# Optimization experiments

Measured on AMD Instinct MI355X. Metric: run time of the kernel, lower is better.

The kernel has to match this reference:

```python
import jax, jax.numpy as jnp
import numpy as np

B, C, H, W_SP = 32, 128, 56, 56
OC, K, STRIDE, PAD = 256, 3, 1, 1


def setup_inputs() -> dict:
    key = jax.random.key(0)
    k1, k2, k3 = jax.random.split(key, 3)
    x = jax.random.normal(k1, (B, C, H, W_SP), dtype=jnp.float32)
    # nn.Linear weight: [out_features, in_features] = [OC, C*K*K]
    W = jax.random.normal(k2, (OC, C * K * K), dtype=jnp.float32) * 0.02
    b = jax.random.normal(k3, (OC,), dtype=jnp.float32) * 0.02
    return {"x": x, "W": W, "b": b}


def reference(x, W, b):
    # The torch module does im2col (unfold+permute+reshape) then Linear.
    # Patch layout after view/permute is (C, kh, kw) flattened, so the
    # Linear weight reshaped to [OC, C, K, K] is exactly an OIHW conv
    # kernel; direct convolution computes identical math without
    # materializing the im2col tensor.
    kernel = W.reshape(OC, C, K, K)
    out = jax.lax.conv_general_dilated(
        x, kernel,
        window_strides=(STRIDE, STRIDE),
        padding=[(PAD, PAD), (PAD, PAD)],
        dimension_numbers=("NCHW", "OIHW", "NCHW"),
    )
    return out + b[None, :, None, None]
```

## Files before the change

kernel.cpp:

```cpp
#include <hip/hip_runtime.h>
#include <hip/hip_bf16.h>
#include <stdint.h>

typedef unsigned short u16;
typedef unsigned int   u32;
typedef __bf16 bf16x8 __attribute__((ext_vector_type(8)));
typedef float  f32x4  __attribute__((ext_vector_type(4)));

#define BATCH 32
#define CIN   128
#define HH    56
#define WW    56
#define OC    256
#define HP    58
#define WP    58
#define PLANE  (HH*WW)
#define KDIM   1152
#define NKT    36

#define XPAD_ELEMS (BATCH*HP*WP*CIN)
#define W3_ELEMS   (OC*KDIM)

#define GLDS16(g, l) __builtin_amdgcn_global_load_lds( \
    (const __attribute__((address_space(1))) void*)(g), \
    (__attribute__((address_space(3))) void*)(l), 16, 0, 0)

__global__ void zero_ws(uint4* __restrict__ p, int n4) {
    int i = blockIdx.x * blockDim.x + threadIdx.x;
    if (i < n4) p[i] = (uint4){0, 0, 0, 0};
}

__global__ __launch_bounds__(256) void pad_tr(const float* __restrict__ x,
                                              u16* __restrict__ xpad) {
    __shared__ u16 T16[56 * 130];
    const int h = blockIdx.x;
    const int b = blockIdx.y;
    const int tid = threadIdx.x;

    const float* src = x + (size_t)b * CIN * PLANE + h * WW;
#pragma unroll
    for (int j = 0; j < 28; ++j) {
        int flat = j * 256 + tid;
        int c = flat / 56;
        int w = flat - c * 56;
        float v = src[(size_t)c * PLANE + w];
        __hip_bfloat16 bv = __float2bfloat16(v);
        T16[w * 130 + c] = *(u16*)&bv;
    }
    __syncthreads();

    const u32* T32 = (const u32*)T16;
    uint4* dst = (uint4*)(xpad + ((size_t)(b * HP + h + 1) * WP + 1) * CIN);
#pragma unroll
    for (int j = 0; j < 4; ++j) {
        int g = j * 256 + tid;
        if (g < 896) {
            int wp = g >> 4, cq = g & 15;
            uint4 v;
            v.x = T32[wp * 65 + cq * 4 + 0];
            v.y = T32[wp * 65 + cq * 4 + 1];
            v.z = T32[wp * 65 + cq * 4 + 2];
            v.w = T32[wp * 65 + cq * 4 + 3];
            dst[g] = v;
        }
    }
}

__global__ void pack_w(const float* __restrict__ W, u16* __restrict__ w3) {
    int o = blockIdx.x * blockDim.x + threadIdx.x;
    if (o >= W3_ELEMS) return;
    int nt   = o / (NKT * 4096);
    int rem  = o - nt * (NKT * 4096);
    int kt   = rem / 4096;
    int rem2 = rem - kt * 4096;
    int ni   = rem2 >> 5;
    int ci   = rem2 & 31;
    int n = nt * 128 + ni;
    int r = kt >> 2;
    int c = ((kt & 3) << 5) + ci;
    float val = W[n * KDIM + c * 9 + r];
    __hip_bfloat16 bv = __float2bfloat16(val);
    w3[o] = *(u16*)&bv;
}

__global__ __launch_bounds__(256) void conv_main(
    const u16* __restrict__ xpad,
    const u16* __restrict__ w3,
    const float* __restrict__ bias,
    float* __restrict__ out)
{
    __shared__ __align__(16) u16 As[128 * 32];
    __shared__ __align__(16) u16 Bs[128 * 32];

    const int tid  = threadIdx.x;
    const int lane = tid & 63;
    const int wv   = tid >> 6;
    const int m0   = blockIdx.x * 128;
    const int nt   = blockIdx.y;

    const int mi0 = wv * 32 + (lane >> 2);
    size_t bbase[2];
#pragma unroll
    for (int i = 0; i < 2; ++i) {
        int mi = mi0 + i * 16;
        int m  = m0 + mi;
        int bb = m / PLANE;
        int s  = m - bb * PLANE;
        int hh = s / WW;
        int ww = s - hh * WW;
        bbase[i] = ((size_t)((bb * HP + hh) * WP + ww) * CIN + (lane & 3) * 8) * 2;
    }
    const char* w3t  = (const char*)(w3 + (size_t)nt * (NKT * 4096));
    const size_t abase = (size_t)(wv * 128 + lane) * 16;

    char* AsW = (char*)As + wv * 2048;
    char* BsW = (char*)Bs + wv * 2048;

    const int wn = wv >> 1, wm = wv & 1;
    const int l16 = lane & 15, quad = lane >> 4;

    f32x4 acc[4][4];
#pragma unroll
    for (int f = 0; f < 4; ++f) {
        f32x4 bv = *(const f32x4*)&bias[nt * 128 + wn * 64 + f * 16 + quad * 4];
#pragma unroll
        for (int g = 0; g < 4; ++g) acc[f][g] = bv;
    }

    for (int r = 0; r < 9; ++r) {
        const int kh = (r * 11) >> 5;
        const int kw = r - kh * 3;
        const size_t xoff = (size_t)(kh * WP + kw) * CIN * 2;
#pragma unroll
        for (int cc = 0; cc < 4; ++cc) {
            const int kt = r * 4 + cc;
#pragma unroll
            for (int i = 0; i < 2; ++i) {
                GLDS16(w3t + (size_t)kt * 8192 + abase + i * 1024,
                       AsW + i * 1024);
                GLDS16((const char*)xpad + bbase[i] + xoff + cc * 64,
                       BsW + i * 1024);
            }
            __syncthreads();

            bf16x8 af[4], bfr[4];
#pragma unroll
            for (int f = 0; f < 4; ++f)
                af[f] = *(const bf16x8*)&As[(wn * 64 + f * 16 + l16) * 32 + quad * 8];
#pragma unroll
            for (int g = 0; g < 4; ++g)
                bfr[g] = *(const bf16x8*)&Bs[(wm * 64 + g * 16 + l16) * 32 + quad * 8];

#pragma unroll
            for (int f = 0; f < 4; ++f)
#pragma unroll
                for (int g = 0; g < 4; ++g)
                    acc[f][g] = __builtin_amdgcn_mfma_f32_16x16x32_bf16(
                        af[f], bfr[g], acc[f][g], 0, 0, 0);
            __syncthreads();
        }
    }

    const int n0 = nt * 128 + wn * 64;
#pragma unroll
    for (int g = 0; g < 4; ++g) {
        const int mm = m0 + wm * 64 + g * 16 + l16;
        const int bb = mm / PLANE;
        const int ss = mm - bb * PLANE;
        float* obase = out + (size_t)bb * (OC * PLANE) + ss;
#pragma unroll
        for (int f = 0; f < 4; ++f) {
#pragma unroll
            for (int i = 0; i < 4; ++i) {
                const int n = n0 + f * 16 + quad * 4 + i;
                obase[(size_t)n * PLANE] = acc[f][g][i];
            }
        }
    }
}

extern "C" void kernel_launch(void* const* d_in, const int* in_sizes, int n_in,
                              void* d_out, int out_size, void* d_ws, size_t ws_size,
                              hipStream_t stream) {
    const float* x    = (const float*)d_in[0];
    const float* W    = (const float*)d_in[1];
    const float* bias = (const float*)d_in[2];
    float* out = (float*)d_out;

    u16* xpad = (u16*)d_ws;
    u16* w3   = xpad + XPAD_ELEMS;

    const int n4 = (XPAD_ELEMS * 2) / 16;
    zero_ws<<<(n4 + 255) / 256, 256, 0, stream>>>((uint4*)xpad, n4);
    pad_tr<<<dim3(HH, BATCH), 256, 0, stream>>>(x, xpad);
    pack_w<<<(W3_ELEMS + 255) / 256, 256, 0, stream>>>(W, w3);

    dim3 grid(784, 2);
    conv_main<<<grid, 256, 0, stream>>>(xpad, w3, bias, out);
}
```

Baseline: 227.0 us.

## Double-buffer conv LDS tiles, swizzle LDS layout, and zero only padding borders

The main conv loop now uses two LDS buffers, so the global-to-LDS loads for the next K tile are issued before the MFMAs on the current tile, and one barrier per iteration is dropped. The LDS rows use an XOR-style chunk rotation to reduce bank conflicts on the bf16x8 fragment reads. The full-workspace zero kernel is replaced by one that clears only the top and bottom padded rows, while pad_tr writes the left and right zero columns itself. This removes a large memory write pass, at the cost of a more complex indexing scheme and doubled LDS use.

```diff
diff --git a/kernel.cpp b/kernel.cpp
--- a/kernel.cpp
+++ b/kernel.cpp
@@ -25,9 +25,14 @@
     (const __attribute__((address_space(1))) void*)(g), \
     (__attribute__((address_space(3))) void*)(l), 16, 0, 0)
 
-__global__ void zero_ws(uint4* __restrict__ p, int n4) {
-    int i = blockIdx.x * blockDim.x + threadIdx.x;
-    if (i < n4) p[i] = (uint4){0, 0, 0, 0};
+__global__ void zero_border(uint4* __restrict__ xp4) {
+    int i = blockIdx.x * 256 + threadIdx.x;
+    if (i >= 64 * 928) return;
+    int row = i / 928;
+    int off = i - row * 928;
+    int b = row >> 1;
+    int h = (row & 1) ? (HP - 1) : 0;
+    xp4[((size_t)(b * HP + h) * WP * CIN) / 8 + off] = (uint4){0, 0, 0, 0};
 }
 
 __global__ __launch_bounds__(256) void pad_tr(const float* __restrict__ x,
@@ -50,17 +55,20 @@
     __syncthreads();
 
     const u32* T32 = (const u32*)T16;
-    uint4* dst = (uint4*)(xpad + ((size_t)(b * HP + h + 1) * WP + 1) * CIN);
+    uint4* dst = (uint4*)(xpad + (size_t)(b * HP + h + 1) * WP * CIN);
 #pragma unroll
     for (int j = 0; j < 4; ++j) {
         int g = j * 256 + tid;
-        if (g < 896) {
+        if (g < 928) {
             int wp = g >> 4, cq = g & 15;
-            uint4 v;
-            v.x = T32[wp * 65 + cq * 4 + 0];
-            v.y = T32[wp * 65 + cq * 4 + 1];
-            v.z = T32[wp * 65 + cq * 4 + 2];
-            v.w = T32[wp * 65 + cq * 4 + 3];
+            uint4 v = (uint4){0, 0, 0, 0};
+            if (wp >= 1 && wp <= 56) {
+                int w = wp - 1;
+                v.x = T32[w * 65 + cq * 4 + 0];
+                v.y = T32[w * 65 + cq * 4 + 1];
+                v.z = T32[w * 65 + cq * 4 + 2];
+                v.w = T32[w * 65 + cq * 4 + 3];
+            }
             dst[g] = v;
         }
     }
@@ -89,8 +97,8 @@
     const float* __restrict__ bias,
     float* __restrict__ out)
 {
-    __shared__ __align__(16) u16 As[128 * 32];
-    __shared__ __align__(16) u16 Bs[128 * 32];
+    __shared__ __align__(16) u16 As[2][128 * 32];
+    __shared__ __align__(16) u16 Bs[2][128 * 32];
 
     const int tid  = threadIdx.x;
     const int lane = tid & 63;
@@ -98,27 +106,38 @@
     const int m0   = blockIdx.x * 128;
     const int nt   = blockIdx.y;
 
-    const int mi0 = wv * 32 + (lane >> 2);
-    size_t bbase[2];
+    const int srow = lane >> 2;
+    const int sc   = lane & 3;
+    size_t abase[2], bbase[2];
 #pragma unroll
     for (int i = 0; i < 2; ++i) {
-        int mi = mi0 + i * 16;
-        int m  = m0 + mi;
+        int rowid = wv * 32 + i * 16 + srow;
+        int q = (sc - ((rowid >> 1) & 3)) & 3;
+        abase[i] = (size_t)rowid * 64 + q * 16;
+        int m  = m0 + rowid;
         int bb = m / PLANE;
         int s  = m - bb * PLANE;
         int hh = s / WW;
         int ww = s - hh * WW;
-        bbase[i] = ((size_t)((bb * HP + hh) * WP + ww) * CIN + (lane & 3) * 8) * 2;
-    }
-    const char* w3t  = (const char*)(w3 + (size_t)nt * (NKT * 4096));
-    const size_t abase = (size_t)(wv * 128 + lane) * 16;
-
-    char* AsW = (char*)As + wv * 2048;
-    char* BsW = (char*)Bs + wv * 2048;
+        bbase[i] = ((size_t)((bb * HP + hh) * WP + ww) * CIN) * 2 + q * 16;
+    }
+    const char* w3t = (const char*)(w3 + (size_t)nt * (NKT * 4096));
+    const char* xb  = (const char*)xpad;
+    char* AsW[2] = { (char*)As[0] + wv * 2048, (char*)As[1] + wv * 2048 };
+    char* BsW[2] = { (char*)Bs[0] + wv * 2048, (char*)Bs[1] + wv * 2048 };
 
     const int wn = wv >> 1, wm = wv & 1;
     const int l16 = lane & 15, quad = lane >> 4;
 
+    int aoff[4], boff[4];
+#pragma unroll
+    for (int f = 0; f < 4; ++f) {
+        int ra = wn * 64 + f * 16 + l16;
+        aoff[f] = ra * 64 + ((quad + (ra >> 1)) & 3) * 16;
+        int rb = wm * 64 + f * 16 + l16;
+        boff[f] = rb * 64 + ((quad + (rb >> 1)) & 3) * 16;
+    }
+
     f32x4 acc[4][4];
 #pragma unroll
     for (int f = 0; f < 4; ++f) {
@@ -127,38 +146,42 @@
         for (int g = 0; g < 4; ++g) acc[f][g] = bv;
     }
 
-    for (int r = 0; r < 9; ++r) {
-        const int kh = (r * 11) >> 5;
+    auto issue = [&](int kt) {
+        const int buf = kt & 1;
+        const int r  = kt >> 2;
+        const int cc = kt & 3;
+        const int kh = r / 3;
         const int kw = r - kh * 3;
-        const size_t xoff = (size_t)(kh * WP + kw) * CIN * 2;
-#pragma unroll
-        for (int cc = 0; cc < 4; ++cc) {
-            const int kt = r * 4 + cc;
-#pragma unroll
-            for (int i = 0; i < 2; ++i) {
-                GLDS16(w3t + (size_t)kt * 8192 + abase + i * 1024,
-                       AsW + i * 1024);
-                GLDS16((const char*)xpad + bbase[i] + xoff + cc * 64,
-                       BsW + i * 1024);
-            }
-            __syncthreads();
-
-            bf16x8 af[4], bfr[4];
-#pragma unroll
-            for (int f = 0; f < 4; ++f)
-                af[f] = *(const bf16x8*)&As[(wn * 64 + f * 16 + l16) * 32 + quad * 8];
+        const size_t xoff = ((size_t)(kh * WP + kw) * CIN + cc * 32) * 2;
+#pragma unroll
+        for (int i = 0; i < 2; ++i) {
+            GLDS16(w3t + (size_t)kt * 8192 + abase[i], AsW[buf] + i * 1024);
+            GLDS16(xb + bbase[i] + xoff,               BsW[buf] + i * 1024);
+        }
+    };
+
+    issue(0);
+#pragma unroll
+    for (int kt = 0; kt < NKT; ++kt) {
+        __syncthreads();
+        if (kt + 1 < NKT) issue(kt + 1);
+
+        const char* Ab = (const char*)As[kt & 1];
+        const char* Bb = (const char*)Bs[kt & 1];
+        bf16x8 af[4], bfr[4];
+#pragma unroll
+        for (int f = 0; f < 4; ++f)
+            af[f] = *(const bf16x8*)(Ab + aoff[f]);
+#pragma unroll
+        for (int g = 0; g < 4; ++g)
+            bfr[g] = *(const bf16x8*)(Bb + boff[g]);
+
+#pragma unroll
+        for (int f = 0; f < 4; ++f)
 #pragma unroll
             for (int g = 0; g < 4; ++g)
-                bfr[g] = *(const bf16x8*)&Bs[(wm * 64 + g * 16 + l16) * 32 + quad * 8];
-
-#pragma unroll
-            for (int f = 0; f < 4; ++f)
-#pragma unroll
-                for (int g = 0; g < 4; ++g)
-                    acc[f][g] = __builtin_amdgcn_mfma_f32_16x16x32_bf16(
-                        af[f], bfr[g], acc[f][g], 0, 0, 0);
-            __syncthreads();
-        }
+                acc[f][g] = __builtin_amdgcn_mfma_f32_16x16x32_bf16(
+                    af[f], bfr[g], acc[f][g], 0, 0, 0);
     }
 
     const int n0 = nt * 128 + wn * 64;
@@ -190,8 +213,7 @@
     u16* xpad = (u16*)d_ws;
     u16* w3   = xpad + XPAD_ELEMS;
 
-    const int n4 = (XPAD_ELEMS * 2) / 16;
-    zero_ws<<<(n4 + 255) / 256, 256, 0, stream>>>((uint4*)xpad, n4);
+    zero_border<<<232, 256, 0, stream>>>((uint4*)xpad);
     pad_tr<<<dim3(HH, BATCH), 256, 0, stream>>>(x, xpad);
     pack_w<<<(W3_ELEMS + 255) / 256, 256, 0, stream>>>(W, w3);
 
```

After: 215.1 us. 5.2% less time.
